# Optimization experiments

Hardware: AMD Instinct MI355X
Metric: run time of the kernel (lower is better)

## Reference

```python
import jax, jax.numpy as jnp
import numpy as np
from jax import lax

B_SZ = 64
D_MODEL = 768
D_INNER = 1536   # expand * d_model
D_STATE = 16
D_CONV = 4
DT_RANK = 48     # ceil(768/16)
ROWS, COLS = 16, 16
L = ROWS * COLS
LN_EPS = 1e-5


def setup_inputs() -> dict:
    key = jax.random.key(0)
    ks = jax.random.split(key, 16)
    def nrm(k, shape, s):
        return jax.random.normal(k, shape, jnp.float32) * s
    # A_log init as in Mamba: log(arange(1..d_state)) tiled over d_inner
    A_log = jnp.log(jnp.tile(jnp.arange(1, D_STATE + 1, dtype=jnp.float32)[None, :], (D_INNER, 1)))
    # dt bias init: inverse-softplus of dt ~ LogUniform(1e-3, 1e-1)
    def dt_bias_init(k):
        u = jax.random.uniform(k, (D_INNER,), jnp.float32)
        dt = jnp.exp(u * (np.log(0.1) - np.log(0.001)) + np.log(0.001))
        return dt + jnp.log(-jnp.expm1(-dt))
    dt_std = DT_RANK ** -0.5
    return {
        "hidden_states": jax.random.normal(ks[0], (B_SZ, L, D_MODEL), jnp.float32),
        "in_proj_w": nrm(ks[1], (2 * D_INNER, D_MODEL), 0.02),
        "conv_w": nrm(ks[2], (D_INNER, D_CONV), 0.2),
        "conv_bias": nrm(ks[3], (D_INNER,), 0.1),
        "conv_w_b": nrm(ks[4], (D_INNER, D_CONV), 0.2),
        "conv_bias_b": nrm(ks[5], (D_INNER,), 0.1),
        "x_proj_w": nrm(ks[6], (DT_RANK + 2 * D_STATE, D_INNER), 0.02),
        "x_proj_w_b": nrm(ks[7], (DT_RANK + 2 * D_STATE, D_INNER), 0.02),
        "dt_proj_w": jax.random.uniform(ks[8], (D_INNER, DT_RANK), jnp.float32, -dt_std, dt_std),
        "dt_proj_w_b": jax.random.uniform(ks[9], (D_INNER, DT_RANK), jnp.float32, -dt_std, dt_std),
        "dt_bias": dt_bias_init(ks[10]),
        "dt_bias_b": dt_bias_init(ks[11]),
        "A_log": A_log,
        "A_b_log": A_log,
        "Dp": jnp.ones((D_INNER,), jnp.float32),
        "Dp_b": jnp.ones((D_INNER,), jnp.float32),
        "ln_gamma": jnp.ones((D_INNER,), jnp.float32),
        "ln_beta": jnp.zeros((D_INNER,), jnp.float32),
        "out_proj_w": nrm(ks[12], (D_MODEL, D_INNER), 0.02),
    }


def _causal_conv_silu(x, w, b):
    # x: (B, D, L); depthwise causal conv (left-pad K-1) + SiLU
    y = lax.conv_general_dilated(x, w[:, None, :], (1,), [(D_CONV - 1, 0)],
                                 dimension_numbers=("NCH", "OIH", "NCH"),
                                 feature_group_count=D_INNER)
    return jax.nn.silu(y + b[None, :, None])


def _selective_scan(u, dt, A_log, Bm, Cm, dt_bias):
    # u, dt: (B, D, Lr); Bm, Cm: (B, N, Lr)
    A = -jnp.exp(A_log)                                     # (D, N)
    delta = jax.nn.softplus(dt + dt_bias[None, :, None])    # (B, D, Lr)
    dA = jnp.exp(jnp.einsum("bdl,dn->lbdn", delta, A))     # (Lr, B, D, N)
    dBu = jnp.einsum("bdl,bnl,bdl->lbdn", delta, Bm, u)    # (Lr, B, D, N)
    C_l = jnp.moveaxis(Cm, -1, 0)                           # (Lr, B, N)
    def step(h, inp):
        dA_t, dBu_t, C_t = inp
        h = dA_t * h + dBu_t
        return h, jnp.einsum("bdn,bn->bd", h, C_t)
    h0 = jnp.zeros(dA.shape[1:], dA.dtype)
    _, ys = lax.scan(step, h0, (dA, dBu, C_l))
    return jnp.moveaxis(ys, 0, -1)                          # (B, D, Lr)


def _direction(x, conv_w, conv_bias, x_proj_w, dt_proj_w, dt_bias, A_log, Dp):
    xc = _causal_conv_silu(x, conv_w, conv_bias)            # (B, D, L)
    x_comp = xc.reshape(-1, D_INNER, ROWS, COLS).mean(axis=3)  # (B, D, ROWS)
    x_dbl = jnp.einsum("bdl,ed->ble", x_comp, x_proj_w)    # (B, ROWS, R+2N)
    dt, Bm, Cm = jnp.split(x_dbl, [DT_RANK, DT_RANK + D_STATE], axis=-1)
    dt = jnp.einsum("blr,dr->bdl", dt, dt_proj_w)          # (B, D, ROWS)
    Bm = jnp.moveaxis(Bm, 1, 2)                             # (B, N, ROWS)
    Cm = jnp.moveaxis(Cm, 1, 2)
    y = _selective_scan(x_comp, dt, A_log, Bm, Cm, dt_bias)
    return jnp.repeat(y, COLS, axis=2) + Dp[None, :, None] * xc  # (B, D, L)


def reference(hidden_states, in_proj_w, conv_w, conv_bias, conv_w_b, conv_bias_b,
              x_proj_w, x_proj_w_b, dt_proj_w, dt_proj_w_b, dt_bias, dt_bias_b,
              A_log, A_b_log, Dp, Dp_b, ln_gamma, ln_beta, out_proj_w):
    xz = jnp.einsum("bld,ed->bel", hidden_states, in_proj_w)  # (B, 2*Di, L)
    x, z = jnp.split(xz, 2, axis=1)
    out_f = _direction(x, conv_w, conv_bias, x_proj_w, dt_proj_w, dt_bias, A_log, Dp)
    out_b = _direction(x[:, :, ::-1], conv_w_b, conv_bias_b, x_proj_w_b, dt_proj_w_b, dt_bias_b, A_b_log, Dp_b)
    comb = jnp.moveaxis((out_f + out_b[:, :, ::-1]) * 0.5, 1, 2)  # (B, L, Di)
    mu = comb.mean(-1, keepdims=True)
    var = comb.var(-1, keepdims=True)
    normed = (comb - mu) * lax.rsqrt(var + LN_EPS) * ln_gamma + ln_beta
    gated = normed * jax.nn.silu(jnp.moveaxis(z, 1, 2))
    return jnp.einsum("bld,od->blo", gated, out_proj_w)       # (B, L, d_model)
```

## Files before the change

### kernel.cpp

```cpp
#include <hip/hip_runtime.h>
#include <cstdint>
#include <cstddef>

typedef __bf16 bf16_t;
typedef __attribute__((ext_vector_type(2))) __bf16 bf16x2;
typedef __attribute__((ext_vector_type(8))) __bf16 bf16x8;
typedef __attribute__((ext_vector_type(4))) float f32x4;

#define NB     64
#define LSEQ   256
#define DM     768
#define DI     1536
#define NSTATE 16
#define NROWS  16
#define RANK   48

#define BF16_PROBE 0x3F803F80u

__device__ __forceinline__ float bf2f(bf16_t v) { return (float)v; }

__device__ __forceinline__ float ldp(const void* p, size_t i, bool isbf) {
  return isbf ? (float)((const bf16_t*)p)[i] : ((const float*)p)[i];
}

__device__ __forceinline__ float silu_f(float x) {
  const float e = __expf(-fabsf(x));
  return (x >= 0.f) ? (x / (1.f + e)) : (x * e / (1.f + e));
}

__device__ __forceinline__ void async16(const bf16_t* g, bf16_t* l) {
  __builtin_amdgcn_global_load_lds(
      (const __attribute__((address_space(1))) void*)g,
      (__attribute__((address_space(3))) void*)l, 16, 0, 0);
}

__global__ __launch_bounds__(256) void cvt_kernel(
    const void* __restrict__ in, bf16_t* __restrict__ out, int n8,
    const uint32_t* __restrict__ probe)
{
  const int i = blockIdx.x * 256 + threadIdx.x;
  if (i >= n8) return;
  if (probe[0] == BF16_PROBE) {
    ((bf16x8*)out)[i] = ((const bf16x8*)in)[i];
  } else {
    const float* f = (const float*)in + (size_t)i * 8;
    f32x4 lo = *(const f32x4*)f, hi = *(const f32x4*)(f + 4);
    ((bf16x8*)out)[i] = (bf16x8){(bf16_t)lo.x, (bf16_t)lo.y, (bf16_t)lo.z, (bf16_t)lo.w,
                                 (bf16_t)hi.x, (bf16_t)hi.y, (bf16_t)hi.z, (bf16_t)hi.w};
  }
}

__global__ __launch_bounds__(256) void gemm_bt_kernel(
    const bf16_t* __restrict__ A, const bf16_t* __restrict__ B,
    void* __restrict__ C, int M, int N, int K, int cIsF32)
{
  __shared__ bf16_t As[128 * 64];
  __shared__ bf16_t Bs[128 * 64];
  const int tid  = threadIdx.x;
  const int wave = tid >> 6;
  const int lane = tid & 63;
  const size_t bm = (size_t)blockIdx.y * 128;
  const size_t bn = (size_t)blockIdx.x * 128;
  const int wm = (wave >> 1) * 64;
  const int wn = (wave & 1) * 64;

  const int src_rr  = lane >> 3;
  const int src_col = ((lane & 7) ^ src_rr) * 8;

  f32x4 acc[4][4];
#pragma unroll
  for (int i = 0; i < 4; i++)
#pragma unroll
    for (int j = 0; j < 4; j++) acc[i][j] = (f32x4){0.f, 0.f, 0.f, 0.f};

  for (int k0 = 0; k0 < K; k0 += 64) {
#pragma unroll
    for (int j = 0; j < 4; j++) {
      const int c = wave * 4 + j;
      const size_t row = c * 8 + src_rr;
      async16(A + (bm + row) * (size_t)K + k0 + src_col, &As[c * 512]);
      async16(B + (bn + row) * (size_t)K + k0 + src_col, &Bs[c * 512]);
    }
    __syncthreads();
#pragma unroll
    for (int s = 0; s < 2; s++) {
      const int r    = lane & 15;
      const int quad = lane >> 4;
      const int r7   = lane & 7;
      const int slot = ((s * 4 + quad) ^ r7) * 8;
      bf16x8 af[4], bfr[4];
#pragma unroll
      for (int mt = 0; mt < 4; mt++)
        af[mt] = *(const bf16x8*)&As[(wm + mt * 16 + r) * 64 + slot];
#pragma unroll
      for (int nt = 0; nt < 4; nt++)
        bfr[nt] = *(const bf16x8*)&Bs[(wn + nt * 16 + r) * 64 + slot];
#pragma unroll
      for (int mt = 0; mt < 4; mt++)
#pragma unroll
        for (int nt = 0; nt < 4; nt++)
          acc[mt][nt] = __builtin_amdgcn_mfma_f32_16x16x32_bf16(
              af[mt], bfr[nt], acc[mt][nt], 0, 0, 0);
    }
    __syncthreads();
  }

  const int col = lane & 15;
  const int rb  = (lane >> 4) * 4;
#pragma unroll
  for (int mt = 0; mt < 4; mt++)
#pragma unroll
    for (int nt = 0; nt < 4; nt++)
#pragma unroll
      for (int r = 0; r < 4; r++) {
        const size_t m = bm + wm + mt * 16 + rb + r;
        const size_t n = bn + wn + nt * 16 + col;
        const size_t ci = m * (size_t)N + n;
        if (cIsF32) ((float*)C)[ci] = acc[mt][nt][r];
        else        ((bf16_t*)C)[ci] = (bf16_t)acc[mt][nt][r];
      }
}

__global__ __launch_bounds__(256) void conv_kernel(
    const bf16_t* __restrict__ xz,
    const void* __restrict__ cw_f, const void* __restrict__ cb_f,
    const void* __restrict__ cw_b, const void* __restrict__ cb_b,
    bf16_t* __restrict__ xc_f, bf16_t* __restrict__ xc_b,
    float* __restrict__ comp_f, float* __restrict__ comp_b,
    const uint32_t* __restrict__ probe)
{
  const bool isbf = (probe[0] == BF16_PROBE);
  const int dir = blockIdx.y;
  int bi = blockIdx.x;
  const int chunk = bi & 3;
  bi >>= 2;
  const int b = bi / 3;
  const int pblk = bi % 3;
  const int d0 = (pblk * 256 + threadIdx.x) * 2;
  const void* cw = dir ? cw_b : cw_f;
  const void* cb = dir ? cb_b : cb_f;
  bf16_t* xc = dir ? xc_b : xc_f;
  float* comp = dir ? comp_b : comp_f;

  const float w00 = ldp(cw, d0 * 4 + 0, isbf), w01 = ldp(cw, d0 * 4 + 1, isbf),
              w02 = ldp(cw, d0 * 4 + 2, isbf), w03 = ldp(cw, d0 * 4 + 3, isbf);
  const float w10 = ldp(cw, (d0 + 1) * 4 + 0, isbf), w11 = ldp(cw, (d0 + 1) * 4 + 1, isbf),
              w12 = ldp(cw, (d0 + 1) * 4 + 2, isbf), w13 = ldp(cw, (d0 + 1) * 4 + 3, isbf);
  const float bias0 = ldp(cb, d0, isbf), bias1 = ldp(cb, d0 + 1, isbf);

  float a3 = 0.f, a2 = 0.f, a1 = 0.f;
  float c3 = 0.f, c2 = 0.f, c1 = 0.f;
  const int lr0 = chunk * 64;
  if (lr0 >= 3) {
#pragma unroll
    for (int i = 3; i >= 1; --i) {
      const int lrp = lr0 - i;
      const int l = dir ? (LSEQ - 1 - lrp) : lrp;
      bf16x2 xv = *(const bf16x2*)(xz + ((size_t)b * LSEQ + l) * (2 * DI) + d0);
      a3 = a2; a2 = a1; a1 = (float)xv.x;
      c3 = c2; c2 = c1; c1 = (float)xv.y;
    }
  }

  float s0 = 0.f, s1 = 0.f;
  for (int lr = lr0; lr < lr0 + 64; ++lr) {
    const int l = dir ? (LSEQ - 1 - lr) : lr;
    bf16x2 xv = *(const bf16x2*)(xz + ((size_t)b * LSEQ + l) * (2 * DI) + d0);
    const float x0 = (float)xv.x, x1 = (float)xv.y;
    float y0 = silu_f(bias0 + w00 * a3 + w01 * a2 + w02 * a1 + w03 * x0);
    float y1 = silu_f(bias1 + w10 * c3 + w11 * c2 + w12 * c1 + w13 * x1);
    a3 = a2; a2 = a1; a1 = x0;
    c3 = c2; c2 = c1; c1 = x1;
    *(bf16x2*)(xc + ((size_t)b * LSEQ + lr) * DI + d0) = (bf16x2){(bf16_t)y0, (bf16_t)y1};
    s0 += y0; s1 += y1;
    if ((lr & 15) == 15) {
      size_t ci = ((size_t)b * NROWS + (lr >> 4)) * DI + d0;
      comp[ci]     = s0 * (1.f / 16.f);
      comp[ci + 1] = s1 * (1.f / 16.f);
      s0 = 0.f; s1 = 0.f;
    }
  }
}

__global__ __launch_bounds__(256) void xproj_kernel(
    const float* __restrict__ comp_f, const float* __restrict__ comp_b,
    const void* __restrict__ w_f, const void* __restrict__ w_b,
    float* __restrict__ xd_f, float* __restrict__ xd_b,
    const uint32_t* __restrict__ probe)
{
  const bool isbf = (probe[0] == BF16_PROBE);
  const int dir = blockIdx.y;
  const int row = blockIdx.x;
  const float* comp = dir ? comp_b : comp_f;
  const void* W = dir ? w_b : w_f;
  float* out = dir ? xd_b : xd_f;

  __shared__ float xrow[DI];
  for (int i = threadIdx.x; i < DI; i += 256) xrow[i] = comp[(size_t)row * DI + i];
  __syncthreads();

  const int wave = threadIdx.x >> 6, lane = threadIdx.x & 63;
  for (int oo = 0; oo < 20; ++oo) {
    const int o = wave * 20 + oo;
    float s = 0.f;
#pragma unroll
    for (int j = 0; j < 24; ++j) {
      const int k = lane + 64 * j;
      s += xrow[k] * ldp(W, (size_t)o * DI + k, isbf);
    }
    for (int off = 32; off; off >>= 1) s += __shfl_down(s, off);
    if (lane == 0) out[(size_t)row * 80 + o] = s;
  }
}

__global__ __launch_bounds__(256) void scan_kernel(
    const float* __restrict__ xd_fg, const float* __restrict__ xd_bg,
    const float* comp_f, const float* comp_b,
    const void* __restrict__ dtw_f, const void* __restrict__ dtw_b,
    const void* __restrict__ dtb_f, const void* __restrict__ dtb_b,
    const void* __restrict__ Al_f, const void* __restrict__ Al_b,
    float* y_fg, float* y_bg,
    const uint32_t* __restrict__ probe)
{
  const bool isbf = (probe[0] == BF16_PROBE);
  const int dir = blockIdx.y;
  const int b = blockIdx.x / 6;
  const int d = (blockIdx.x % 6) * 256 + threadIdx.x;
  const float* xd_g = dir ? xd_bg : xd_fg;
  const float* comp = dir ? comp_b : comp_f;
  const void* dtw = dir ? dtw_b : dtw_f;
  const void* dtb = dir ? dtb_b : dtb_f;
  const void* Al  = dir ? Al_b : Al_f;
  float* y = dir ? y_bg : y_fg;

  __shared__ float xd[NROWS * 80];
  for (int i = threadIdx.x; i < NROWS * 80; i += 256) xd[i] = xd_g[(size_t)b * (NROWS * 80) + i];
  __syncthreads();

  float dt[NROWS];
#pragma unroll
  for (int l = 0; l < NROWS; l++) dt[l] = 0.f;
  for (int r = 0; r < RANK; r++) {
    const float w = ldp(dtw, (size_t)d * RANK + r, isbf);
#pragma unroll
    for (int l = 0; l < NROWS; l++) dt[l] += xd[l * 80 + r] * w;
  }

  float A[NSTATE];
#pragma unroll
  for (int n = 0; n < NSTATE; n++) A[n] = -__expf(ldp(Al, (size_t)d * NSTATE + n, isbf));
  const float bias = ldp(dtb, d, isbf);

  float h[NSTATE];
#pragma unroll
  for (int n = 0; n < NSTATE; n++) h[n] = 0.f;

  for (int l = 0; l < NROWS; l++) {
    const float u = comp[((size_t)b * NROWS + l) * DI + d];
    const float dv = dt[l] + bias;
    const float delta = (dv > 15.f) ? dv : log1pf(__expf(dv));
    const float du = delta * u;
    float yv = 0.f;
#pragma unroll
    for (int n = 0; n < NSTATE; n++) {
      const float hn = __expf(delta * A[n]) * h[n] + du * xd[l * 80 + RANK + n];
      h[n] = hn;
      yv += hn * xd[l * 80 + RANK + NSTATE + n];
    }
    y[((size_t)b * NROWS + l) * DI + d] = yv;
  }
}

__global__ __launch_bounds__(256) void combine_kernel(
    const float* __restrict__ y_f, const float* __restrict__ y_b,
    bf16_t* xcg_f,
    const bf16_t* __restrict__ xc_b,
    const bf16_t* __restrict__ xz,
    const void* __restrict__ Dp, const void* __restrict__ Dp_b,
    const void* __restrict__ gamma, const void* __restrict__ beta,
    const uint32_t* __restrict__ probe)
{
  const bool isbf = (probe[0] == BF16_PROBE);
  const int m = blockIdx.x;
  const int b = m >> 8, l = m & 255;
  const int lr = LSEQ - 1 - l;
  const int tid = threadIdx.x;

  float v[6];
  float sum = 0.f, sq = 0.f;
#pragma unroll
  for (int i = 0; i < 6; i++) {
    const int d = tid + i * 256;
    const float cf = bf2f(xcg_f[((size_t)b * LSEQ + l) * DI + d]);
    const float cb = bf2f(xc_b[((size_t)b * LSEQ + lr) * DI + d]);
    const float vf = y_f[((size_t)b * NROWS + (l >> 4)) * DI + d] + ldp(Dp, d, isbf) * cf;
    const float vb = y_b[((size_t)b * NROWS + (lr >> 4)) * DI + d] + ldp(Dp_b, d, isbf) * cb;
    const float c = 0.5f * (vf + vb);
    v[i] = c; sum += c; sq += c * c;
  }
  for (int off = 32; off; off >>= 1) {
    sum += __shfl_down(sum, off);
    sq  += __shfl_down(sq, off);
  }
  __shared__ float rs[4], rq[4];
  if ((tid & 63) == 0) { rs[tid >> 6] = sum; rq[tid >> 6] = sq; }
  __syncthreads();
  const float S  = rs[0] + rs[1] + rs[2] + rs[3];
  const float SQ = rq[0] + rq[1] + rq[2] + rq[3];
  const float mu = S * (1.f / (float)DI);
  const float var = fmaxf(SQ * (1.f / (float)DI) - mu * mu, 0.f);
  const float rstd = rsqrtf(var + 1e-5f);
#pragma unroll
  for (int i = 0; i < 6; i++) {
    const int d = tid + i * 256;
    const float nrm = (v[i] - mu) * rstd * ldp(gamma, d, isbf) + ldp(beta, d, isbf);
    const float z = bf2f(xz[((size_t)b * LSEQ + l) * (2 * DI) + DI + d]);
    xcg_f[(size_t)m * DI + d] = (bf16_t)(nrm * silu_f(z));
  }
}

extern "C" void kernel_launch(void* const* d_in, const int* in_sizes, int n_in,
                              void* d_out, int out_size, void* d_ws, size_t ws_size,
                              hipStream_t stream)
{
  (void)in_sizes; (void)n_in; (void)out_size; (void)ws_size;
  const void* H     = d_in[0];
  const void* Win   = d_in[1];
  const void* cw_f  = d_in[2];
  const void* cb_f  = d_in[3];
  const void* cw_b  = d_in[4];
  const void* cb_b  = d_in[5];
  const void* xpw_f = d_in[6];
  const void* xpw_b = d_in[7];
  const void* dtw_f = d_in[8];
  const void* dtw_b = d_in[9];
  const void* dtb_f = d_in[10];
  const void* dtb_b = d_in[11];
  const void* Al_f  = d_in[12];
  const void* Al_b  = d_in[13];
  const void* Dp    = d_in[14];
  const void* Dp_b  = d_in[15];
  const void* gam   = d_in[16];
  const void* bet   = d_in[17];
  const void* Wout  = d_in[18];
  const uint32_t* probe = (const uint32_t*)d_in[14];

  const size_t M = (size_t)NB * LSEQ;
  char* ws = (char*)d_ws;
  bf16_t* xz    = (bf16_t*)ws;  ws += M * (2 * DI) * sizeof(bf16_t);
  bf16_t* xc_f  = (bf16_t*)ws;  ws += M * DI * sizeof(bf16_t);
  bf16_t* xc_b  = (bf16_t*)ws;  ws += M * DI * sizeof(bf16_t);
  float* comp_f = (float*)ws;   ws += (size_t)NB * NROWS * DI * sizeof(float);
  float* comp_b = (float*)ws;   ws += (size_t)NB * NROWS * DI * sizeof(float);
  float* xd_f   = (float*)ws;   ws += (size_t)NB * NROWS * 80 * sizeof(float);
  float* xd_b   = (float*)ws;   ws += (size_t)NB * NROWS * 80 * sizeof(float);
  bf16_t* Hb    = (bf16_t*)ws;  ws += M * DM * sizeof(bf16_t);
  bf16_t* Winb  = (bf16_t*)ws;  ws += (size_t)(2 * DI) * DM * sizeof(bf16_t);
  bf16_t* Woutb = (bf16_t*)ws;  ws += (size_t)DM * DI * sizeof(bf16_t);

  cvt_kernel<<<(int)((M * DM / 8 + 255) / 256), 256, 0, stream>>>(H, Hb, (int)(M * DM / 8), probe);
  cvt_kernel<<<(2 * DI * DM / 8 + 255) / 256, 256, 0, stream>>>(Win, Winb, 2 * DI * DM / 8, probe);
  cvt_kernel<<<(DM * DI / 8 + 255) / 256, 256, 0, stream>>>(Wout, Woutb, DM * DI / 8, probe);

  gemm_bt_kernel<<<dim3(2 * DI / 128, M / 128), 256, 0, stream>>>(
      Hb, Winb, xz, (int)M, 2 * DI, DM, 0);

  conv_kernel<<<dim3(768, 2), 256, 0, stream>>>(
      xz, cw_f, cb_f, cw_b, cb_b, xc_f, xc_b, comp_f, comp_b, probe);

  xproj_kernel<<<dim3(NB * NROWS, 2), 256, 0, stream>>>(
      comp_f, comp_b, xpw_f, xpw_b, xd_f, xd_b, probe);

  scan_kernel<<<dim3(NB * (DI / 256), 2), 256, 0, stream>>>(
      xd_f, xd_b, comp_f, comp_b, dtw_f, dtw_b, dtb_f, dtb_b, Al_f, Al_b,
      comp_f, comp_b, probe);

  combine_kernel<<<dim3(NB * LSEQ), 256, 0, stream>>>(
      comp_f, comp_b, xc_f, xc_b, xz, Dp, Dp_b, gam, bet, probe);

  gemm_bt_kernel<<<dim3(DM / 128, M / 128), 256, 0, stream>>>(
      xc_f, Woutb, d_out, (int)M, DM, DI, 1);
}
```

Measured before the change: 516.1 us.

## Replace GEMM with 256x256 tiled, double-buffered, 8-wave pipelined MFMA kernel

The 128x128 single-buffered GEMM is replaced by a 256x256-tile kernel with 512 threads. It double-buffers LDS (128 KB) using async global-to-LDS loads interleaved with MFMA phases, adds s_setprio around the MFMA clusters, and remaps workgroups with an XCD-aware swizzle. The goal is to hide global load latency and raise data reuse per tile for both projection GEMMs. The cost is much more LDS and register pressure, and a hand-written waitcnt/barrier schedule that is fragile.

Result: faster. 478.1 us (-7.4%).

```diff
diff --git a/kernel.cpp b/kernel.cpp
--- a/kernel.cpp
+++ b/kernel.cpp
@@ -50,74 +50,138 @@
   }
 }
 
-__global__ __launch_bounds__(256) void gemm_bt_kernel(
+#define LDS_IDX(ab, db, half) (((ab) << 2) + ((db) << 1) + (half))
+
+#define STAGE(ab, db, half, kt) do {                                          \
+    const int _kt = ((kt) < NT) ? (kt) : (NT - 1);                            \
+    const bf16_t* _g = (ab) ? B : A;                                          \
+    const size_t _rb = ((ab) ? bn : bm) + (size_t)((half) * 128);             \
+    bf16_t* _l = &sm[LDS_IDX(ab, db, half)][0];                               \
+    _Pragma("unroll")                                                         \
+    for (int _j = 0; _j < 2; _j++) {                                          \
+      const int _c = wave * 2 + _j;                                           \
+      async16(_g + (_rb + _c * 8 + srow) * (size_t)K + (size_t)_kt * 64 + scol,\
+              _l + _c * 512);                                                 \
+    }                                                                         \
+  } while (0)
+
+#define LOAD_A(db, mg) do {                                                   \
+    _Pragma("unroll")                                                         \
+    for (int _t = 0; _t < 2; _t++) {                                          \
+      const int _mt = (mg) * 2 + _t;                                          \
+      const int _lr = _mt * 32 + wm * 16 + r;                                 \
+      const bf16_t* _b = &sm[LDS_IDX(0, db, _mt >> 2)][(_lr & 127) * 64];     \
+      _Pragma("unroll")                                                       \
+      for (int _s = 0; _s < 2; _s++)                                          \
+        af[_t][_s] = *(const bf16x8*)&_b[(((_s * 4 + quad) ^ r7) * 8)];       \
+    }                                                                         \
+  } while (0)
+
+#define LOAD_B(db) do {                                                       \
+    _Pragma("unroll")                                                         \
+    for (int _nt = 0; _nt < 4; _nt++) {                                       \
+      const int _lr = _nt * 64 + wn * 16 + r;                                 \
+      const bf16_t* _b = &sm[LDS_IDX(1, db, _lr >> 7)][(_lr & 127) * 64];     \
+      _Pragma("unroll")                                                       \
+      for (int _s = 0; _s < 2; _s++)                                          \
+        bfr[_nt][_s] = *(const bf16x8*)&_b[(((_s * 4 + quad) ^ r7) * 8)];     \
+    }                                                                         \
+  } while (0)
+
+#define MFMA16(mg) do {                                                       \
+    __builtin_amdgcn_s_setprio(1);                                            \
+    _Pragma("unroll")                                                         \
+    for (int _t = 0; _t < 2; _t++)                                            \
+    _Pragma("unroll")                                                         \
+    for (int _nt = 0; _nt < 4; _nt++)                                         \
+    _Pragma("unroll")                                                         \
+    for (int _s = 0; _s < 2; _s++)                                            \
+      acc[(mg) * 2 + _t][_nt] = __builtin_amdgcn_mfma_f32_16x16x32_bf16(      \
+          af[_t][_s], bfr[_nt][_s], acc[(mg) * 2 + _t][_nt], 0, 0, 0);        \
+    __builtin_amdgcn_s_setprio(0);                                            \
+  } while (0)
+
+#define BAR()    __builtin_amdgcn_s_barrier()
+#define WAITL0() asm volatile("s_waitcnt lgkmcnt(0)" ::: "memory")
+#define WAITV6() asm volatile("s_waitcnt vmcnt(6)" ::: "memory")
+
+__global__ __launch_bounds__(512, 2) void gemm256_kernel(
     const bf16_t* __restrict__ A, const bf16_t* __restrict__ B,
     void* __restrict__ C, int M, int N, int K, int cIsF32)
 {
-  __shared__ bf16_t As[128 * 64];
-  __shared__ bf16_t Bs[128 * 64];
+  __shared__ bf16_t sm[8][8192];
   const int tid  = threadIdx.x;
-  const int wave = tid >> 6;
-  const int lane = tid & 63;
-  const size_t bm = (size_t)blockIdx.y * 128;
-  const size_t bn = (size_t)blockIdx.x * 128;
-  const int wm = (wave >> 1) * 64;
-  const int wn = (wave & 1) * 64;
-
-  const int src_rr  = lane >> 3;
-  const int src_col = ((lane & 7) ^ src_rr) * 8;
-
-  f32x4 acc[4][4];
-#pragma unroll
-  for (int i = 0; i < 4; i++)
+  const int wave = tid >> 6, lane = tid & 63;
+  const int wm = wave >> 2, wn = wave & 3;
+  const int r = lane & 15, quad = lane >> 4, r7 = lane & 7;
+  const int srow = lane >> 3;
+  const int scol = ((lane & 7) ^ srow) * 8;
+  const int NT = K >> 6;
+
+  const int nwg  = gridDim.x * gridDim.y;
+  const int orig = blockIdx.y * gridDim.x + blockIdx.x;
+  const int swz  = (orig & 7) * (nwg >> 3) + (orig >> 3);
+  const size_t bm = (size_t)(swz / gridDim.x) * 256;
+  const size_t bn = (size_t)(swz % gridDim.x) * 256;
+
+  f32x4 acc[8][4];
+#pragma unroll
+  for (int i = 0; i < 8; i++)
 #pragma unroll
     for (int j = 0; j < 4; j++) acc[i][j] = (f32x4){0.f, 0.f, 0.f, 0.f};
 
-  for (int k0 = 0; k0 < K; k0 += 64) {
-#pragma unroll
-    for (int j = 0; j < 4; j++) {
-      const int c = wave * 4 + j;
-      const size_t row = c * 8 + src_rr;
-      async16(A + (bm + row) * (size_t)K + k0 + src_col, &As[c * 512]);
-      async16(B + (bn + row) * (size_t)K + k0 + src_col, &Bs[c * 512]);
-    }
-    __syncthreads();
-#pragma unroll
-    for (int s = 0; s < 2; s++) {
-      const int r    = lane & 15;
-      const int quad = lane >> 4;
-      const int r7   = lane & 7;
-      const int slot = ((s * 4 + quad) ^ r7) * 8;
-      bf16x8 af[4], bfr[4];
-#pragma unroll
-      for (int mt = 0; mt < 4; mt++)
-        af[mt] = *(const bf16x8*)&As[(wm + mt * 16 + r) * 64 + slot];
-#pragma unroll
-      for (int nt = 0; nt < 4; nt++)
-        bfr[nt] = *(const bf16x8*)&Bs[(wn + nt * 16 + r) * 64 + slot];
-#pragma unroll
-      for (int mt = 0; mt < 4; mt++)
-#pragma unroll
-        for (int nt = 0; nt < 4; nt++)
-          acc[mt][nt] = __builtin_amdgcn_mfma_f32_16x16x32_bf16(
-              af[mt], bfr[nt], acc[mt][nt], 0, 0, 0);
-    }
-    __syncthreads();
+  bf16x8 af[2][2];
+  bf16x8 bfr[4][2];
+
+  STAGE(1, 0, 0, 0);  STAGE(1, 0, 1, 0);  STAGE(0, 0, 0, 0);  STAGE(0, 0, 1, 0);
+  asm volatile("s_waitcnt vmcnt(4)" ::: "memory");
+  STAGE(1, 1, 0, 1);  STAGE(1, 1, 1, 1);  STAGE(0, 1, 0, 1);
+  WAITV6();
+  BAR();
+
+  const int NP = NT >> 1;
+  for (int i = 0; i < NP; ++i) {
+    const int t1 = 2 * i + 1, t2 = 2 * i + 2, t3 = 2 * i + 3;
+    LOAD_B(0); LOAD_A(0, 0); STAGE(0, 1, 1, t1);
+    BAR(); WAITL0(); MFMA16(0); BAR();
+
+    LOAD_A(0, 1); STAGE(1, 0, 0, t2);
+    BAR(); WAITL0(); MFMA16(1); BAR();
+
+    LOAD_A(0, 2); STAGE(1, 0, 1, t2);
+    BAR(); WAITL0(); MFMA16(2); BAR();
+
+    LOAD_A(0, 3); STAGE(0, 0, 0, t2);
+    WAITV6();
+    BAR(); WAITL0(); MFMA16(3); BAR();
+
+    LOAD_B(1); LOAD_A(1, 0); STAGE(0, 0, 1, t2);
+    BAR(); WAITL0(); MFMA16(0); BAR();
+
+    LOAD_A(1, 1); STAGE(1, 1, 0, t3);
+    BAR(); WAITL0(); MFMA16(1); BAR();
+
+    LOAD_A(1, 2); STAGE(1, 1, 1, t3);
+    BAR(); WAITL0(); MFMA16(2); BAR();
+
+    LOAD_A(1, 3); STAGE(0, 1, 0, t3);
+    WAITV6();
+    BAR(); WAITL0(); MFMA16(3); BAR();
   }
 
   const int col = lane & 15;
-  const int rb  = (lane >> 4) * 4;
-#pragma unroll
-  for (int mt = 0; mt < 4; mt++)
+  const int rb4 = quad * 4;
+#pragma unroll
+  for (int mt = 0; mt < 8; mt++)
 #pragma unroll
     for (int nt = 0; nt < 4; nt++)
 #pragma unroll
-      for (int r = 0; r < 4; r++) {
-        const size_t m = bm + wm + mt * 16 + rb + r;
-        const size_t n = bn + wn + nt * 16 + col;
+      for (int v = 0; v < 4; v++) {
+        const size_t m = bm + mt * 32 + wm * 16 + rb4 + v;
+        const size_t n = bn + nt * 64 + wn * 16 + col;
         const size_t ci = m * (size_t)N + n;
-        if (cIsF32) ((float*)C)[ci] = acc[mt][nt][r];
-        else        ((bf16_t*)C)[ci] = (bf16_t)acc[mt][nt][r];
+        if (cIsF32) ((float*)C)[ci] = acc[mt][nt][v];
+        else        ((bf16_t*)C)[ci] = (bf16_t)acc[mt][nt][v];
       }
 }
 
@@ -362,7 +426,7 @@
   cvt_kernel<<<(2 * DI * DM / 8 + 255) / 256, 256, 0, stream>>>(Win, Winb, 2 * DI * DM / 8, probe);
   cvt_kernel<<<(DM * DI / 8 + 255) / 256, 256, 0, stream>>>(Wout, Woutb, DM * DI / 8, probe);
 
-  gemm_bt_kernel<<<dim3(2 * DI / 128, M / 128), 256, 0, stream>>>(
+  gemm256_kernel<<<dim3(2 * DI / 256, M / 256), 512, 0, stream>>>(
       Hb, Winb, xz, (int)M, 2 * DI, DM, 0);
 
   conv_kernel<<<dim3(768, 2), 256, 0, stream>>>(
@@ -378,6 +442,6 @@
   combine_kernel<<<dim3(NB * LSEQ), 256, 0, stream>>>(
       comp_f, comp_b, xc_f, xc_b, xz, Dp, Dp_b, gam, bet, probe);
 
-  gemm_bt_kernel<<<dim3(DM / 128, M / 128), 256, 0, stream>>>(
+  gemm256_kernel<<<dim3(DM / 256, M / 256), 512, 0, stream>>>(
       xc_f, Woutb, d_out, (int)M, DM, DI, 1);
 }
```
